# Kernel tuning notes

Hardware: AMD Instinct MI355X
Metric: run time of the kernel (lower is better)

Reference implementation:

```python
import jax, jax.numpy as jnp
import numpy as np

POOL_LEN = 2
POOL_SIZE = 4  # pool_len**2
NUM_ITERS = 3

def pool_grid(pool_size):
    # grid of relative positions inside the pooling block, row-major, centered at 0
    b = int(np.sqrt(pool_size))
    off = np.arange(b, dtype=np.float32) - (b - 1) / 2.0
    hh, ww = np.meshgrid(off, off, indexing='ij')
    return jnp.asarray(np.stack([hh.ravel(), ww.ravel()], -1))  # (pool_size, 2)

def posevec_to_rotmat(p):
    # p = (cos t, sin t) unit vector -> [[c,-s],[s,c]]
    x, y = p[..., 0], p[..., 1]
    return jnp.stack([jnp.stack([x, -y], -1), jnp.stack([y, x], -1)], -2)

def inverse_pose(p):
    return jnp.stack([p[..., 0], -p[..., 1]], -1)

def space_to_depth(x, b):
    # x: (B,H,W,D,P) -> (B,H/b,W/b,b*b*D,P), depth ordered (h_in_block, w_in_block, d)
    B, H, W, D, P = x.shape
    x = x.reshape(B, H // b, b, W // b, b, D, P).transpose(0, 1, 3, 2, 4, 5, 6)
    return x.reshape(B, H // b, W // b, b * b * D, P)

def capsule_forward(x, a, pose, alpha, beta, lin_w, lin_b, tg1_w, tg2_w):
    B, H, W, Cin = a.shape
    Cout = lin_w.shape[0]
    b, P = POOL_LEN, POOL_SIZE
    Hp, Wp = (H + 1) // b, (W + 1) // b
    a4 = space_to_depth(a[..., None], b)[..., 0].reshape(B, Hp, Wp, P, Cin)
    pose4 = space_to_depth(pose, b).reshape(B, Hp, Wp, P, Cin, 2)
    # mean_per_channel: sum over pool positions, normalize with zero-norm guard
    m = pose4.sum(3)                                            # (B,Hp,Wp,Cin,2)
    n = jnp.linalg.norm(m, axis=-1, keepdims=True)
    means = m / (n + (1.0 - jnp.sign(n)))
    # get_votes: rotate pool positions into the mean frame, generate per-pair thetas
    pp = pool_grid(P).reshape(1, 1, 1, P, 1, 2, 1)
    rot = posevec_to_rotmat(inverse_pose(means))[:, :, :, None]  # (B,Hp,Wp,1,Cin,2,2)
    tpos = jnp.matmul(rot, pp)                                   # (B,Hp,Wp,P,Cin,2,1)
    tpos = jax.lax.stop_gradient(tpos).reshape(-1, Cin * 2)      # detach(); (B*Hp*Wp*P, 2Cin)
    theta = (tpos @ tg1_w.T) @ tg2_w.T                           # (N, Cout*Cin)
    theta = theta.reshape(B, Hp, Wp, P, Cout, Cin).transpose(0, 1, 2, 4, 3, 5)
    s, c = jnp.sin(theta), jnp.cos(theta)
    g = jnp.stack([c, -s, s, c], -1).reshape(B, Hp, Wp, Cout, P, Cin, 2, 2)
    pm = posevec_to_rotmat(pose4[:, :, :, None])                 # (B,Hp,Wp,1,P,Cin,2,2)
    vote = jnp.matmul(pm, g)[..., 0].reshape(B, Hp, Wp, Cout, P * Cin, 2)

    def mean_fn(v, w):
        mu = (v * w[..., None]).sum(-2)                          # (B,Hp,Wp,Cout,2)
        msk = jnp.sign(jnp.abs(mu))                              # elementwise, as original
        return mu / (jnp.linalg.norm(mu, axis=-1, keepdims=True) + (1.0 - msk))

    def dist(p, v):
        return (1.0 - (p[..., None, :] * v).sum(-1)) / 2.0

    a_e = jnp.broadcast_to(a4.reshape(B, Hp, Wp, 1, P * Cin), (B, Hp, Wp, Cout, P * Cin))
    weight = a_e
    pose_o = mean_fn(vote, weight)
    for _ in range(NUM_ITERS):
        weight = (1.0 - dist(pose_o, vote)) * a_e
        pose_o = mean_fn(vote, weight)
    nd = (1.0 - dist(pose_o, vote)) * weight
    w_sum = jnp.sign(jnp.abs(weight)).sum(-1)
    msk = jnp.sign(jnp.abs(w_sum))
    nd = nd.sum(-1) / (w_sum + (1.0 - msk)) * msk
    agreement = jax.nn.sigmoid(alpha.reshape(1, 1, 1, -1) * nd + (beta.reshape(1, 1, 1, -1) - 1.0)) * msk
    # feature max-pool + linear
    xp = space_to_depth(x[..., None], b)[..., 0].reshape(B, Hp, Wp, P, Cin).max(-2)
    xp = xp.reshape(-1, Cin)
    x_out = xp @ lin_w.T + lin_b
    return x_out, agreement, pose_o, xp

def setup_inputs():
    key = jax.random.key(0)
    ks = jax.random.split(key, 8)
    B, H, W, Cin, Cout = 8, 32, 32, 32, 64
    x = jax.random.normal(ks[0], (B, H, W, Cin), jnp.float32)
    a = jax.random.uniform(ks[1], (B, H, W, Cin), jnp.float32)
    pose = jax.random.normal(ks[2], (B, H, W, Cin, 2), jnp.float32)
    pose = pose / jnp.linalg.norm(pose, axis=-1, keepdims=True)  # unit pose vectors
    alpha = jnp.ones((1,), jnp.float32)
    beta = jnp.ones((1,), jnp.float32)
    lin_w = jax.random.normal(ks[3], (Cout, Cin), jnp.float32) * 0.1
    lin_b = jax.random.normal(ks[4], (Cout,), jnp.float32) * 0.1
    tg1_w = jax.random.normal(ks[5], (32, 2 * Cin), jnp.float32) * 0.1
    tg2_w = jax.random.normal(ks[6], (Cout * Cin, 32), jnp.float32) * 0.1
    return {"x": x, "a": a, "pose": pose, "alpha": alpha, "beta": beta,
            "lin_w": lin_w, "lin_b": lin_b, "tg1_w": tg1_w, "tg2_w": tg2_w}

def reference(x, a, pose, alpha, beta, lin_w, lin_b, tg1_w, tg2_w):
    return capsule_forward(x, a, pose, alpha, beta, lin_w, lin_b, tg1_w, tg2_w)
```

## Files before the change

kernel.cpp:

```cpp
#include <hip/hip_runtime.h>
#include <math.h>

#define NSITE 2048

#define OFF_XOUT 0
#define OFF_AGR  (NSITE*64)
#define OFF_POSE (OFF_AGR + NSITE*64)
#define OFF_XP   (OFF_POSE + NSITE*128)

#define WS_META_OFF (NSITE*128)

__device__ __forceinline__ void norm2_guard(float x, float y, float* ox, float* oy) {
    const float n2  = x*x + y*y;
    const float inv = (n2 > 0.f) ? rsqrtf(n2) : 0.f;
    *ox = x*inv; *oy = y*inv;
}

__global__ __launch_bounds__(256) void capsA(
    const float* __restrict__ x, const float* __restrict__ a,
    const float* __restrict__ pose,
    const float* __restrict__ tg1, const float* __restrict__ lin_w,
    const float* __restrict__ lin_b, float* __restrict__ out,
    float* __restrict__ ws)
{
    const int wave = threadIdx.x >> 6, lane = threadIdx.x & 63;
    const int s  = blockIdx.x*4 + wave;
    const int b  = s >> 8, hp = (s >> 4) & 15, wp = s & 15;
    const int ci = lane & 31, p0 = lane >> 5;

    __shared__ float stp[4][4][64];
    __shared__ float xps[4][32];

    const int base = ((b*32 + 2*hp)*32 + 2*wp)*32 + ci;
    const int i0 = base + p0*32;
    const int i1 = base + 1024 + p0*32;
    const float2 pe0 = ((const float2*)pose)[i0];
    const float2 pe1 = ((const float2*)pose)[i1];
    const float  x0  = x[i0], x1 = x[i1];
    const float  a0  = a[i0], a1 = a[i1];

    const float o0x = __shfl_xor(pe0.x, 32, 64);
    const float o0y = __shfl_xor(pe0.y, 32, 64);
    const float o1x = __shfl_xor(pe1.x, 32, 64);
    const float o1y = __shfl_xor(pe1.y, 32, 64);
    const bool first = (p0 == 0);
    const float A0x = first ? pe0.x : o0x,  A1x = first ? o0x : pe0.x;
    const float A2x = first ? pe1.x : o1x,  A3x = first ? o1x : pe1.x;
    const float A0y = first ? pe0.y : o0y,  A1y = first ? o0y : pe0.y;
    const float A2y = first ? pe1.y : o1y,  A3y = first ? o1y : pe1.y;
    float mx = ((A0x + A1x) + A2x) + A3x;
    float my = ((A0y + A1y) + A2y) + A3y;

    float xm = fmaxf(x0, x1);
    xm = fmaxf(xm, __shfl_xor(xm, 32, 64));
    float sa  = a0 + a1;
    float cnt = (a0 != 0.f ? 1.f : 0.f) + (a1 != 0.f ? 1.f : 0.f);
    sa  += __shfl_xor(sa,  32, 64);
    cnt += __shfl_xor(cnt, 32, 64);
    #pragma unroll
    for (int m = 1; m <= 16; m <<= 1) {
        sa  += __shfl_xor(sa,  m, 64);
        cnt += __shfl_xor(cnt, m, 64);
    }
    if (lane == 0) ((float2*)(ws + WS_META_OFF))[s] = make_float2(sa, cnt);
    if (p0 == 0) {
        out[OFF_XP + s*32 + ci] = xm;
        xps[wave][ci] = xm;
    }

    {
        const float n   = sqrtf(mx*mx + my*my);
        const float den = n + (n == 0.f ? 1.f : 0.f);
        mx /= den; my /= den;
    }

    {
        const float ww_ = (float)p0 - 0.5f;
        const float t0x = -0.5f*mx + my*ww_;
        const float t0y =  0.5f*my + mx*ww_;
        const float t1x =  0.5f*mx + my*ww_;
        const float t1y = -0.5f*my + mx*ww_;
        ((float2*)stp[wave][p0    ])[ci] = make_float2(t0x, t0y);
        ((float2*)stp[wave][p0 + 2])[ci] = make_float2(t1x, t1y);
    }
    __syncthreads();

    {
        const float4* w4 = (const float4*)(tg1 + ci*64);
        const float4* r0 = (const float4*)stp[wave][p0];
        const float4* r1 = (const float4*)stp[wave][p0 + 2];
        float h0 = 0.f, h1 = 0.f;
        #pragma unroll
        for (int k = 0; k < 16; ++k) {
            const float4 wv = w4[k], u = r0[k], v = r1[k];
            h0 += wv.x*u.x + wv.y*u.y + wv.z*u.z + wv.w*u.w;
            h1 += wv.x*v.x + wv.y*v.y + wv.z*v.z + wv.w*v.w;
        }
        ws[s*128 + p0*32 + ci]       = h0;
        ws[s*128 + (p0 + 2)*32 + ci] = h1;
    }

    {
        float acc = lin_b[lane];
        const float4* lw = (const float4*)(lin_w + lane*32);
        const float4* xv = (const float4*)xps[wave];
        #pragma unroll
        for (int k = 0; k < 8; ++k) {
            const float4 wv = lw[k], u = xv[k];
            acc += wv.x*u.x + wv.y*u.y + wv.z*u.z + wv.w*u.w;
        }
        out[OFF_XOUT + s*64 + lane] = acc;
    }
}

__global__ __launch_bounds__(256, 8) void capsB(
    const float* __restrict__ a, const float* __restrict__ pose,
    const float* __restrict__ tg2, const float* __restrict__ ws,
    const float* __restrict__ alpha, const float* __restrict__ beta,
    float* __restrict__ out)
{
    const int g    = blockIdx.x;
    const int sb   = blockIdx.y;
    const int tid  = threadIdx.x;
    const int wave = tid >> 6, lane = tid & 63;
    const int co   = g*8 + wave*2 + (lane >> 5);
    const int ci   = lane & 31;

    float4 r[8];
    {
        const float4* rp = (const float4*)(tg2 + (co*32 + ci)*32);
        #pragma unroll
        for (int k = 0; k < 8; ++k) r[k] = rp[k];
    }
    const float alp = alpha[0];
    const float bet = beta[0] - 1.0f;
    const float2* ws_meta = (const float2*)(ws + WS_META_OFF);

    const int s0 = sb*2;
    #pragma unroll
    for (int sl = 0; sl < 2; ++sl) {
        const int s = s0 + sl;
        const float4* h4 = (const float4*)(ws + s*128);
        float th0 = 0.f, th1 = 0.f, th2 = 0.f, th3 = 0.f;
        #pragma unroll
        for (int k = 0; k < 8; ++k) {
            const float4 rk = r[k];
            const float4 ha = h4[k];
            const float4 hb = h4[8  + k];
            const float4 hc = h4[16 + k];
            const float4 hd = h4[24 + k];
            th0 += rk.x*ha.x + rk.y*ha.y + rk.z*ha.z + rk.w*ha.w;
            th1 += rk.x*hb.x + rk.y*hb.y + rk.z*hb.z + rk.w*hb.w;
            th2 += rk.x*hc.x + rk.y*hc.y + rk.z*hc.z + rk.w*hc.w;
            th3 += rk.x*hd.x + rk.y*hd.y + rk.z*hd.z + rk.w*hd.w;
        }
        const float th[4] = {th0, th1, th2, th3};

        const int b   = s >> 8, hpi = (s >> 4) & 15, wpi = s & 15;
        const int base = ((b*32 + 2*hpi)*32 + 2*wpi)*32 + ci;

        float Sx = 0.f, Sy = 0.f, Sxx = 0.f, Sxy = 0.f, Syy = 0.f;
        #pragma unroll
        for (int p = 0; p < 4; ++p) {
            const int idx = base + (p >> 1)*1024 + (p & 1)*32;
            const float2 pe = ((const float2*)pose)[idx];
            const float  av = a[idx];
            float sn, cs;
            __sincosf(th[p], &sn, &cs);
            const float vx = pe.x*cs - pe.y*sn;
            const float vy = pe.y*cs + pe.x*sn;
            const float ax = av*vx, ay = av*vy;
            Sx += ax; Sy += ay;
            Sxx += ax*vx; Sxy += ax*vy; Syy += ay*vy;
        }
        #pragma unroll
        for (int m = 1; m <= 16; m <<= 1) {
            Sx  += __shfl_xor(Sx,  m, 64);
            Sy  += __shfl_xor(Sy,  m, 64);
            Sxx += __shfl_xor(Sxx, m, 64);
            Sxy += __shfl_xor(Sxy, m, 64);
            Syy += __shfl_xor(Syy, m, 64);
        }

        float px, py;
        norm2_guard(Sx, Sy, &px, &py);
        float qx = px, qy = py;
        #pragma unroll
        for (int it = 0; it < 3; ++it) {
            qx = px; qy = py;
            const float mx = Sx + px*Sxx + py*Sxy;
            const float my = Sy + px*Sxy + py*Syy;
            norm2_guard(mx, my, &px, &py);
        }
        const float2 meta = ws_meta[s];
        const float nd_sum = 0.25f*(meta.x + (px + qx)*Sx + (py + qy)*Sy
                           + px*qx*Sxx + (px*qy + py*qx)*Sxy + py*qy*Syy);
        const float wsum = meta.y;
        const float msk  = (wsum != 0.f) ? 1.f : 0.f;
        const float nd   = nd_sum / (wsum + (1.f - msk)) * msk;
        const float z    = alp*nd + bet;
        const float agr  = msk / (1.f + __expf(-z));

        if ((lane & 31) == 0) {
            out[OFF_AGR  + s*64  + co]       = agr;
            out[OFF_POSE + s*128 + co*2]     = px;
            out[OFF_POSE + s*128 + co*2 + 1] = py;
        }
    }
}

extern "C" void kernel_launch(void* const* d_in, const int* in_sizes, int n_in,
                              void* d_out, int out_size, void* d_ws, size_t ws_size,
                              hipStream_t stream) {
    const float* x     = (const float*)d_in[0];
    const float* a     = (const float*)d_in[1];
    const float* pose  = (const float*)d_in[2];
    const float* alpha = (const float*)d_in[3];
    const float* beta  = (const float*)d_in[4];
    const float* lin_w = (const float*)d_in[5];
    const float* lin_b = (const float*)d_in[6];
    const float* tg1   = (const float*)d_in[7];
    const float* tg2   = (const float*)d_in[8];
    float* out = (float*)d_out;
    float* ws  = (float*)d_ws;

    capsA<<<NSITE/4, 256, 0, stream>>>(x, a, pose, tg1, lin_w, lin_b, out, ws);
    capsB<<<dim3(8, NSITE/2), 256, 0, stream>>>(a, pose, tg2, ws, alpha, beta, out);
}
```

Baseline: 136.0 us.

## Compute theta GEMM with split-bf16 MFMA and exact fp32 fallback for ill-conditioned sites

The theta projection (h @ tg2^T) moves from scalar fp32 dot products to MFMA bf16 instructions, with both operands split into three bf16 parts and six cross-product MFMAs to approximate fp32 accuracy. The main kernel records a flag for each (site, out-channel) whose routing-norm iterates came near zero. A third kernel then recomputes flagged entries with the original fp32 path. This adds a kernel launch, extra workspace traffic for the split operands and flags, and a fallback grid that mostly exits early.

```diff
diff --git a/kernel.cpp b/kernel.cpp
--- a/kernel.cpp
+++ b/kernel.cpp
@@ -9,9 +9,39 @@
 #define OFF_XP   (OFF_POSE + NSITE*128)
 
 #define WS_META_OFF (NSITE*128)
+#define WS_HHI_OFF  266240
+#define WS_HLO_OFF  397312
+#define WS_HZZ_OFF  528384
+#define WS_FLG_OFF  659456
+
+typedef __attribute__((ext_vector_type(8))) short bf16x8;
+typedef __attribute__((ext_vector_type(4))) float f32x4;
+typedef unsigned char uchar;
+
+__device__ __forceinline__ short f2bf(float f) {
+    union { float f; unsigned u; } c; c.f = f;
+    const unsigned r = c.u + 0x7FFF + ((c.u >> 16) & 1);
+    return (short)(r >> 16);
+}
+__device__ __forceinline__ float bf2f(short h) {
+    union { unsigned u; float f; } c; c.u = ((unsigned)(unsigned short)h) << 16;
+    return c.f;
+}
+__device__ __forceinline__ void f2bf_split3(float f, short* hi, short* lo, short* ll) {
+    *hi = f2bf(f);
+    const float r = f - bf2f(*hi);
+    *lo = f2bf(r);
+    *ll = f2bf(r - bf2f(*lo));
+}
 
 __device__ __forceinline__ void norm2_guard(float x, float y, float* ox, float* oy) {
     const float n2  = x*x + y*y;
+    const float inv = (n2 > 0.f) ? rsqrtf(n2) : 0.f;
+    *ox = x*inv; *oy = y*inv;
+}
+__device__ __forceinline__ void norm2_guard_m(float x, float y, float* ox, float* oy, float* minr2) {
+    const float n2  = x*x + y*y;
+    *minr2 = fminf(*minr2, n2);
     const float inv = (n2 > 0.f) ? rsqrtf(n2) : 0.f;
     *ox = x*inv; *oy = y*inv;
 }
@@ -73,7 +103,6 @@
         const float den = n + (n == 0.f ? 1.f : 0.f);
         mx /= den; my /= den;
     }
-
     {
         const float ww_ = (float)p0 - 0.5f;
         const float t0x = -0.5f*mx + my*ww_;
@@ -98,6 +127,17 @@
         }
         ws[s*128 + p0*32 + ci]       = h0;
         ws[s*128 + (p0 + 2)*32 + ci] = h1;
+        short* hhi = (short*)(ws + WS_HHI_OFF);
+        short* hlo = (short*)(ws + WS_HLO_OFF);
+        short* hzz = (short*)(ws + WS_HZZ_OFF);
+        short h0h, h0l, h0z, h1h, h1l, h1z;
+        f2bf_split3(h0, &h0h, &h0l, &h0z);
+        f2bf_split3(h1, &h1h, &h1l, &h1z);
+        const int e0 = s*128 + p0*32 + ci;
+        const int e1 = s*128 + (p0 + 2)*32 + ci;
+        hhi[e0] = h0h; hhi[e1] = h1h;
+        hlo[e0] = h0l; hlo[e1] = h1l;
+        hzz[e0] = h0z; hzz[e1] = h1z;
     }
 
     {
@@ -113,68 +153,91 @@
     }
 }
 
-__global__ __launch_bounds__(256, 8) void capsB(
+__global__ __launch_bounds__(256) void capsB_m(
     const float* __restrict__ a, const float* __restrict__ pose,
-    const float* __restrict__ tg2, const float* __restrict__ ws,
+    const float* __restrict__ tg2, float* __restrict__ ws,
     const float* __restrict__ alpha, const float* __restrict__ beta,
     float* __restrict__ out)
 {
-    const int g    = blockIdx.x;
-    const int sb   = blockIdx.y;
+    const int co   = blockIdx.x;
     const int tid  = threadIdx.x;
     const int wave = tid >> 6, lane = tid & 63;
-    const int co   = g*8 + wave*2 + (lane >> 5);
-    const int ci   = lane & 31;
-
-    float4 r[8];
-    {
-        const float4* rp = (const float4*)(tg2 + (co*32 + ci)*32);
-        #pragma unroll
-        for (int k = 0; k < 8; ++k) r[k] = rp[k];
-    }
+    const int q    = lane >> 4;
+    const int n    = lane & 15;
+
+    bf16x8 b0h, b0l, b0z, b1h, b1l, b1z;
+    {
+        const float* r0 = tg2 + (co*32 + n)*32 + q*8;
+        const float* r1 = r0 + 512;
+        #pragma unroll
+        for (int j = 0; j < 8; ++j) {
+            short h, l, z;
+            f2bf_split3(r0[j], &h, &l, &z); b0h[j] = h; b0l[j] = l; b0z[j] = z;
+            f2bf_split3(r1[j], &h, &l, &z); b1h[j] = h; b1l[j] = l; b1z[j] = z;
+        }
+    }
+    const short* hhi = (const short*)(ws + WS_HHI_OFF);
+    const short* hlo = (const short*)(ws + WS_HLO_OFF);
+    const short* hzz = (const short*)(ws + WS_HZZ_OFF);
+    uchar* flags = (uchar*)(ws + WS_FLG_OFF);
     const float alp = alpha[0];
     const float bet = beta[0] - 1.0f;
     const float2* ws_meta = (const float2*)(ws + WS_META_OFF);
 
-    const int s0 = sb*2;
-    #pragma unroll
-    for (int sl = 0; sl < 2; ++sl) {
-        const int s = s0 + sl;
-        const float4* h4 = (const float4*)(ws + s*128);
-        float th0 = 0.f, th1 = 0.f, th2 = 0.f, th3 = 0.f;
-        #pragma unroll
-        for (int k = 0; k < 8; ++k) {
-            const float4 rk = r[k];
-            const float4 ha = h4[k];
-            const float4 hb = h4[8  + k];
-            const float4 hc = h4[16 + k];
-            const float4 hd = h4[24 + k];
-            th0 += rk.x*ha.x + rk.y*ha.y + rk.z*ha.z + rk.w*ha.w;
-            th1 += rk.x*hb.x + rk.y*hb.y + rk.z*hb.z + rk.w*hb.w;
-            th2 += rk.x*hc.x + rk.y*hc.y + rk.z*hc.z + rk.w*hc.w;
-            th3 += rk.x*hd.x + rk.y*hd.y + rk.z*hd.z + rk.w*hd.w;
-        }
-        const float th[4] = {th0, th1, th2, th3};
-
-        const int b   = s >> 8, hpi = (s >> 4) & 15, wpi = s & 15;
-        const int base = ((b*32 + 2*hpi)*32 + 2*wpi)*32 + ci;
+    #pragma unroll
+    for (int it = 0; it < 4; ++it) {
+        const int s0 = (((blockIdx.y*4 + wave)*4) + it)*4;
+
+        const int aoff = (s0 + (n >> 2))*128 + (n & 3)*32 + q*8;
+        const bf16x8 ah = *(const bf16x8*)(hhi + aoff);
+        const bf16x8 al = *(const bf16x8*)(hlo + aoff);
+        const bf16x8 az = *(const bf16x8*)(hzz + aoff);
+
+        f32x4 c0 = {0.f, 0.f, 0.f, 0.f};
+        f32x4 c1 = {0.f, 0.f, 0.f, 0.f};
+        c0 = __builtin_amdgcn_mfma_f32_16x16x32_bf16(az, b0h, c0, 0, 0, 0);
+        c0 = __builtin_amdgcn_mfma_f32_16x16x32_bf16(ah, b0z, c0, 0, 0, 0);
+        c0 = __builtin_amdgcn_mfma_f32_16x16x32_bf16(al, b0l, c0, 0, 0, 0);
+        c0 = __builtin_amdgcn_mfma_f32_16x16x32_bf16(al, b0h, c0, 0, 0, 0);
+        c0 = __builtin_amdgcn_mfma_f32_16x16x32_bf16(ah, b0l, c0, 0, 0, 0);
+        c0 = __builtin_amdgcn_mfma_f32_16x16x32_bf16(ah, b0h, c0, 0, 0, 0);
+        c1 = __builtin_amdgcn_mfma_f32_16x16x32_bf16(az, b1h, c1, 0, 0, 0);
+        c1 = __builtin_amdgcn_mfma_f32_16x16x32_bf16(ah, b1z, c1, 0, 0, 0);
+        c1 = __builtin_amdgcn_mfma_f32_16x16x32_bf16(al, b1l, c1, 0, 0, 0);
+        c1 = __builtin_amdgcn_mfma_f32_16x16x32_bf16(al, b1h, c1, 0, 0, 0);
+        c1 = __builtin_amdgcn_mfma_f32_16x16x32_bf16(ah, b1l, c1, 0, 0, 0);
+        c1 = __builtin_amdgcn_mfma_f32_16x16x32_bf16(ah, b1h, c1, 0, 0, 0);
+
+        const int site = s0 + q;
+        const int b    = site >> 8, hpi = (site >> 4) & 15, wpi = site & 15;
+        const int base = ((b*32 + 2*hpi)*32 + 2*wpi)*32;
 
         float Sx = 0.f, Sy = 0.f, Sxx = 0.f, Sxy = 0.f, Syy = 0.f;
         #pragma unroll
         for (int p = 0; p < 4; ++p) {
-            const int idx = base + (p >> 1)*1024 + (p & 1)*32;
-            const float2 pe = ((const float2*)pose)[idx];
-            const float  av = a[idx];
-            float sn, cs;
-            __sincosf(th[p], &sn, &cs);
-            const float vx = pe.x*cs - pe.y*sn;
-            const float vy = pe.y*cs + pe.x*sn;
-            const float ax = av*vx, ay = av*vy;
-            Sx += ax; Sy += ay;
-            Sxx += ax*vx; Sxy += ax*vy; Syy += ay*vy;
-        }
-        #pragma unroll
-        for (int m = 1; m <= 16; m <<= 1) {
+            const int idx0 = base + (p >> 1)*1024 + (p & 1)*32 + n;
+            const int idx1 = idx0 + 16;
+            const float2 pe0 = ((const float2*)pose)[idx0];
+            const float2 pe1 = ((const float2*)pose)[idx1];
+            const float  a0  = a[idx0];
+            const float  a1  = a[idx1];
+            float s0n, c0n, s1n, c1n;
+            __sincosf(c0[p], &s0n, &c0n);
+            __sincosf(c1[p], &s1n, &c1n);
+            const float v0x = pe0.x*c0n - pe0.y*s0n;
+            const float v0y = pe0.y*c0n + pe0.x*s0n;
+            const float v1x = pe1.x*c1n - pe1.y*s1n;
+            const float v1y = pe1.y*c1n + pe1.x*s1n;
+            const float a0x = a0*v0x, a0y = a0*v0y;
+            const float a1x = a1*v1x, a1y = a1*v1y;
+            Sx  += a0x + a1x;
+            Sy  += a0y + a1y;
+            Sxx += a0x*v0x + a1x*v1x;
+            Sxy += a0x*v0y + a1x*v1y;
+            Syy += a0y*v0y + a1y*v1y;
+        }
+        #pragma unroll
+        for (int m = 1; m <= 8; m <<= 1) {
             Sx  += __shfl_xor(Sx,  m, 64);
             Sy  += __shfl_xor(Sy,  m, 64);
             Sxx += __shfl_xor(Sxx, m, 64);
@@ -182,17 +245,18 @@
             Syy += __shfl_xor(Syy, m, 64);
         }
 
+        float minr2 = 3.4e38f;
         float px, py;
-        norm2_guard(Sx, Sy, &px, &py);
+        norm2_guard_m(Sx, Sy, &px, &py, &minr2);
         float qx = px, qy = py;
         #pragma unroll
-        for (int it = 0; it < 3; ++it) {
+        for (int it2 = 0; it2 < 3; ++it2) {
             qx = px; qy = py;
             const float mx = Sx + px*Sxx + py*Sxy;
             const float my = Sy + px*Sxy + py*Syy;
-            norm2_guard(mx, my, &px, &py);
-        }
-        const float2 meta = ws_meta[s];
+            norm2_guard_m(mx, my, &px, &py, &minr2);
+        }
+        const float2 meta = ws_meta[site];
         const float nd_sum = 0.25f*(meta.x + (px + qx)*Sx + (py + qy)*Sy
                            + px*qx*Sxx + (px*qy + py*qx)*Sxy + py*qy*Syy);
         const float wsum = meta.y;
@@ -200,12 +264,109 @@
         const float nd   = nd_sum / (wsum + (1.f - msk)) * msk;
         const float z    = alp*nd + bet;
         const float agr  = msk / (1.f + __expf(-z));
-
-        if ((lane & 31) == 0) {
-            out[OFF_AGR  + s*64  + co]       = agr;
-            out[OFF_POSE + s*128 + co*2]     = px;
-            out[OFF_POSE + s*128 + co*2 + 1] = py;
-        }
+        const int fl = (minr2 < 2.5e-3f*(meta.x*meta.x)) ? 1 : 0;
+
+        if (n == 0) {
+            out[OFF_AGR  + site*64  + co]       = agr;
+            out[OFF_POSE + site*128 + co*2]     = px;
+            out[OFF_POSE + site*128 + co*2 + 1] = py;
+            flags[site*64 + co] = (uchar)fl;
+        }
+    }
+}
+
+__global__ __launch_bounds__(256) void capsB_fix(
+    const float* __restrict__ a, const float* __restrict__ pose,
+    const float* __restrict__ tg2, const float* __restrict__ ws,
+    const float* __restrict__ alpha, const float* __restrict__ beta,
+    float* __restrict__ out)
+{
+    const int g    = blockIdx.x;
+    const int s    = blockIdx.y;
+    const int tid  = threadIdx.x;
+    const int wave = tid >> 6, lane = tid & 63;
+    const int co   = g*8 + wave*2 + (lane >> 5);
+    const int ci   = lane & 31;
+
+    const uchar* flags = (const uchar*)(ws + WS_FLG_OFF);
+    const bool need = flags[s*64 + co] != 0;
+    if (__ballot(need) == 0ULL) return;
+
+    float4 r[8];
+    {
+        const float4* rp = (const float4*)(tg2 + (co*32 + ci)*32);
+        #pragma unroll
+        for (int k = 0; k < 8; ++k) r[k] = rp[k];
+    }
+    const float alp = alpha[0];
+    const float bet = beta[0] - 1.0f;
+    const float2* ws_meta = (const float2*)(ws + WS_META_OFF);
+
+    const float4* h4 = (const float4*)(ws + s*128);
+    float th0 = 0.f, th1 = 0.f, th2 = 0.f, th3 = 0.f;
+    #pragma unroll
+    for (int k = 0; k < 8; ++k) {
+        const float4 rk = r[k];
+        const float4 ha = h4[k];
+        const float4 hb = h4[8  + k];
+        const float4 hc = h4[16 + k];
+        const float4 hd = h4[24 + k];
+        th0 += rk.x*ha.x + rk.y*ha.y + rk.z*ha.z + rk.w*ha.w;
+        th1 += rk.x*hb.x + rk.y*hb.y + rk.z*hb.z + rk.w*hb.w;
+        th2 += rk.x*hc.x + rk.y*hc.y + rk.z*hc.z + rk.w*hc.w;
+        th3 += rk.x*hd.x + rk.y*hd.y + rk.z*hd.z + rk.w*hd.w;
+    }
+    const float th[4] = {th0, th1, th2, th3};
+
+    const int b   = s >> 8, hpi = (s >> 4) & 15, wpi = s & 15;
+    const int base = ((b*32 + 2*hpi)*32 + 2*wpi)*32 + ci;
+
+    float Sx = 0.f, Sy = 0.f, Sxx = 0.f, Sxy = 0.f, Syy = 0.f;
+    #pragma unroll
+    for (int p = 0; p < 4; ++p) {
+        const int idx = base + (p >> 1)*1024 + (p & 1)*32;
+        const float2 pe = ((const float2*)pose)[idx];
+        const float  av = a[idx];
+        float sn, cs;
+        __sincosf(th[p], &sn, &cs);
+        const float vx = pe.x*cs - pe.y*sn;
+        const float vy = pe.y*cs + pe.x*sn;
+        const float ax = av*vx, ay = av*vy;
+        Sx += ax; Sy += ay;
+        Sxx += ax*vx; Sxy += ax*vy; Syy += ay*vy;
+    }
+    #pragma unroll
+    for (int m = 1; m <= 16; m <<= 1) {
+        Sx  += __shfl_xor(Sx,  m, 64);
+        Sy  += __shfl_xor(Sy,  m, 64);
+        Sxx += __shfl_xor(Sxx, m, 64);
+        Sxy += __shfl_xor(Sxy, m, 64);
+        Syy += __shfl_xor(Syy, m, 64);
+    }
+
+    float px, py;
+    norm2_guard(Sx, Sy, &px, &py);
+    float qx = px, qy = py;
+    #pragma unroll
+    for (int it = 0; it < 3; ++it) {
+        qx = px; qy = py;
+        const float mx = Sx + px*Sxx + py*Sxy;
+        const float my = Sy + px*Sxy + py*Syy;
+        norm2_guard(mx, my, &px, &py);
+    }
+    const float2 meta = ws_meta[s];
+    const float nd_sum = 0.25f*(meta.x + (px + qx)*Sx + (py + qy)*Sy
+                       + px*qx*Sxx + (px*qy + py*qx)*Sxy + py*qy*Syy);
+    const float wsum = meta.y;
+    const float msk  = (wsum != 0.f) ? 1.f : 0.f;
+    const float nd   = nd_sum / (wsum + (1.f - msk)) * msk;
+    const float z    = alp*nd + bet;
+    const float agr  = msk / (1.f + __expf(-z));
+
+    if ((lane & 31) == 0) {
+        out[OFF_AGR  + s*64  + co]       = agr;
+        out[OFF_POSE + s*128 + co*2]     = px;
+        out[OFF_POSE + s*128 + co*2 + 1] = py;
     }
 }
 
@@ -225,5 +386,6 @@
     float* ws  = (float*)d_ws;
 
     capsA<<<NSITE/4, 256, 0, stream>>>(x, a, pose, tg1, lin_w, lin_b, out, ws);
-    capsB<<<dim3(8, NSITE/2), 256, 0, stream>>>(a, pose, tg2, ws, alpha, beta, out);
-}
+    capsB_m<<<dim3(64, 32), 256, 0, stream>>>(a, pose, tg2, ws, alpha, beta, out);
+    capsB_fix<<<dim3(8, NSITE), 256, 0, stream>>>(a, pose, tg2, ws, alpha, beta, out);
+}
```

Result: no change. 134.2 us (-1.3%).
